# Performance work log

Measured on AMD Instinct MI355X. Metric: run time of the kernel, lower is better.

## Reference

```python
import jax, jax.numpy as jnp
import numpy as np

BS, N, D_IN, D_OUT, D_ENC, K = 8, 2048, 128, 128, 128, 2
EPS = 1e-5


def layer_norm(x, g, b):
    m = jnp.mean(x, axis=-1, keepdims=True)
    v = jnp.mean(jnp.square(x - m), axis=-1, keepdims=True)
    return (x - m) * jax.lax.rsqrt(v + EPS) * g + b


def setup_inputs() -> dict:
    key = jax.random.key(0)
    ks = jax.random.split(key, 12)
    s = lambda d: 1.0 / np.sqrt(d)
    return {
        "x": jax.random.normal(ks[0], (BS, N, D_IN), jnp.float32),
        "enc": jax.random.normal(ks[1], (BS, N, D_ENC), jnp.float32),
        "ff_enc_w": jax.random.uniform(ks[2], (D_IN, D_ENC), jnp.float32, -s(D_ENC), s(D_ENC)),
        "ff_enc_b": jax.random.uniform(ks[3], (D_IN,), jnp.float32, -s(D_ENC), s(D_ENC)),
        "ln1_g": jnp.ones((D_IN,), jnp.float32),
        "ln1_b": jnp.zeros((D_IN,), jnp.float32),
        "ln2_g": jnp.ones((D_IN,), jnp.float32),
        "ln2_b": jnp.zeros((D_IN,), jnp.float32),
        "ff0_w": jax.random.uniform(ks[4], (K, D_IN, D_IN), jnp.float32, -s(D_IN), s(D_IN)),
        "ff1_w": jax.random.uniform(ks[5], (K, D_OUT, D_IN), jnp.float32, -s(D_IN), s(D_IN)),
        "attn_w": jax.random.uniform(ks[6], (K, 2 * D_IN), jnp.float32, -s(2 * D_IN), s(2 * D_IN)),
    }


def reference(x, enc, ff_enc_w, ff_enc_b, ln1_g, ln1_b, ln2_g, ln2_b, ff0_w, ff1_w, attn_w):
    # x: [bs, n, d_in]; enc: [bs, n, d_enc]
    x = x + jnp.einsum("bne,de->bnd", enc, ff_enc_w) + ff_enc_b
    x_norm = layer_norm(x, ln1_g, ln1_b)
    k = ff0_w.shape[0]
    h_next = jnp.zeros(x.shape[:2] + (ff1_w.shape[1],), x.dtype)
    atten_agg = jnp.zeros(x.shape[:2] + (x.shape[1],), x.dtype)
    d = x.shape[-1]
    for i in range(k):
        h = jnp.einsum("bnd,ed->bne", x_norm, ff0_w[i])  # [bs,n,d]
        # cat(h_i, h_j) @ a  ==  h_i @ a1 + h_j @ a2  (additive-attention identity)
        s1 = h @ attn_w[i, :d]  # [bs,n]
        s2 = h @ attn_w[i, d:]  # [bs,n]
        e = jax.nn.leaky_relu(s1[:, :, None] + s2[:, None, :], negative_slope=0.01)
        atten = jax.nn.softmax(e, axis=2)  # [bs,n,n], softmax over j
        attentioned = jnp.einsum("bij,bjd->bid", atten, h) + x  # residual
        attentioned = layer_norm(attentioned, ln2_g, ln2_b)
        h_next = h_next + jax.nn.elu(jnp.einsum("bnd,od->bno", attentioned, ff1_w[i])) / k
        atten_agg = atten_agg + jax.lax.stop_gradient(atten) / k
    return (h_next, atten_agg)
```

## Files before the change

kernel.cpp:

```cpp
#include <hip/hip_runtime.h>
#include <hip/hip_bf16.h>
#include <math.h>

#define BSZ 8
#define NSEQ 2048
#define DD 128
#define ROWS (BSZ*NSEQ)
#define EPS 1e-5f

__device__ __forceinline__ float f4get(const float4& v, int i){
    return i==0 ? v.x : i==1 ? v.y : i==2 ? v.z : v.w;
}
__device__ __forceinline__ float eluf(float z){ return z > 0.f ? z : expm1f(z); }

__global__ __launch_bounds__(256) void k_transpose(
    const float* __restrict__ Wenc, const float* __restrict__ ff0,
    const float* __restrict__ ff1, float* __restrict__ Wt)
{
    __shared__ float t[32][33];
    const int m = blockIdx.x >> 4;
    const int tile = blockIdx.x & 15;
    const int ti = tile >> 2, tj = tile & 3;
    const float* src = (m == 0) ? Wenc
                     : (m <= 2) ? ff0 + (size_t)(m-1)*16384
                                : ff1 + (size_t)(m-3)*16384;
    float* dst = Wt + (size_t)m*16384;
    const int c = threadIdx.x & 31, r8 = threadIdx.x >> 5;
    #pragma unroll
    for (int p = 0; p < 4; ++p){
        int r = r8 + p*8;
        t[r][c] = src[(ti*32 + r)*128 + tj*32 + c];
    }
    __syncthreads();
    #pragma unroll
    for (int p = 0; p < 4; ++p){
        int r = r8 + p*8;
        dst[(tj*32 + r)*128 + ti*32 + c] = t[c][r];
    }
}

template<int MODE>
__global__ __launch_bounds__(256) void k_gemm(
    const float* __restrict__ A, const float* __restrict__ Bt,
    float* __restrict__ C,
    const float* __restrict__ P0, const float* __restrict__ P1,
    const float* __restrict__ P2, const float* __restrict__ P3,
    float* __restrict__ O1, float* __restrict__ O2)
{
    __shared__ float As[64][36];
    __shared__ float Bs[32][128];
    const int tid = threadIdx.x;
    const int tx = tid & 15, ty = tid >> 4;
    const int rowBase = blockIdx.x * 64;

    float acc[4][8];
    #pragma unroll
    for (int i = 0; i < 4; ++i)
        #pragma unroll
        for (int j = 0; j < 8; ++j) acc[i][j] = 0.f;

    for (int k0 = 0; k0 < 128; k0 += 32){
        {
            const int kk = tid & 31, rr = tid >> 5;
            #pragma unroll
            for (int p = 0; p < 8; ++p){
                int r = rr + p*8;
                As[r][kk] = A[(size_t)(rowBase + r)*128 + k0 + kk];
            }
        }
        {
            const int n = tid & 127, kk2 = tid >> 7;
            #pragma unroll
            for (int p = 0; p < 16; ++p){
                int kk = kk2 + p*2;
                Bs[kk][n] = Bt[(size_t)(k0 + kk)*128 + n];
            }
        }
        __syncthreads();
        #pragma unroll
        for (int kk4 = 0; kk4 < 32; kk4 += 4){
            float4 a[4];
            float4 b[4][2];
            #pragma unroll
            for (int rr = 0; rr < 4; ++rr)
                a[rr] = *(const float4*)&As[4*ty + rr][kk4];
            #pragma unroll
            for (int kk = 0; kk < 4; ++kk){
                b[kk][0] = *(const float4*)&Bs[kk4 + kk][8*tx];
                b[kk][1] = *(const float4*)&Bs[kk4 + kk][8*tx + 4];
            }
            #pragma unroll
            for (int kk = 0; kk < 4; ++kk){
                float bb[8] = {b[kk][0].x, b[kk][0].y, b[kk][0].z, b[kk][0].w,
                               b[kk][1].x, b[kk][1].y, b[kk][1].z, b[kk][1].w};
                #pragma unroll
                for (int rr = 0; rr < 4; ++rr){
                    float av = f4get(a[rr], kk);
                    #pragma unroll
                    for (int cc = 0; cc < 8; ++cc)
                        acc[rr][cc] += av * bb[cc];
                }
            }
        }
        __syncthreads();
    }

    const int c0 = 8*tx;
    if (MODE == 0){
        float4 be0 = *(const float4*)&P1[c0], be1 = *(const float4*)&P1[c0+4];
        float4 g0  = *(const float4*)&P2[c0], g1v = *(const float4*)&P2[c0+4];
        float4 bb0 = *(const float4*)&P3[c0], bb1 = *(const float4*)&P3[c0+4];
        #pragma unroll
        for (int rr = 0; rr < 4; ++rr){
            const size_t off = (size_t)(rowBase + 4*ty + rr)*128 + c0;
            float4 xi0 = *(const float4*)&P0[off];
            float4 xi1 = *(const float4*)&P0[off+4];
            float v[8];
            v[0]=acc[rr][0]+xi0.x+be0.x; v[1]=acc[rr][1]+xi0.y+be0.y;
            v[2]=acc[rr][2]+xi0.z+be0.z; v[3]=acc[rr][3]+xi0.w+be0.w;
            v[4]=acc[rr][4]+xi1.x+be1.x; v[5]=acc[rr][5]+xi1.y+be1.y;
            v[6]=acc[rr][6]+xi1.z+be1.z; v[7]=acc[rr][7]+xi1.w+be1.w;
            *(float4*)&C[off]   = make_float4(v[0],v[1],v[2],v[3]);
            *(float4*)&C[off+4] = make_float4(v[4],v[5],v[6],v[7]);
            float s = v[0]+v[1]+v[2]+v[3]+v[4]+v[5]+v[6]+v[7];
            #pragma unroll
            for (int m = 1; m < 16; m <<= 1) s += __shfl_xor(s, m, 64);
            float mean = s * (1.f/128.f);
            float q = 0.f;
            #pragma unroll
            for (int j = 0; j < 8; ++j){ float d = v[j]-mean; q += d*d; }
            #pragma unroll
            for (int m = 1; m < 16; m <<= 1) q += __shfl_xor(q, m, 64);
            float rstd = rsqrtf(q * (1.f/128.f) + EPS);
            float o[8];
            o[0]=(v[0]-mean)*rstd*g0.x+bb0.x; o[1]=(v[1]-mean)*rstd*g0.y+bb0.y;
            o[2]=(v[2]-mean)*rstd*g0.z+bb0.z; o[3]=(v[3]-mean)*rstd*g0.w+bb0.w;
            o[4]=(v[4]-mean)*rstd*g1v.x+bb1.x; o[5]=(v[5]-mean)*rstd*g1v.y+bb1.y;
            o[6]=(v[6]-mean)*rstd*g1v.z+bb1.z; o[7]=(v[7]-mean)*rstd*g1v.w+bb1.w;
            *(float4*)&O1[off]   = make_float4(o[0],o[1],o[2],o[3]);
            *(float4*)&O1[off+4] = make_float4(o[4],o[5],o[6],o[7]);
        }
    } else if (MODE == 1 || MODE == 4){
        float4 a10 = *(const float4*)&P1[c0],     a11 = *(const float4*)&P1[c0+4];
        float4 a20 = *(const float4*)&P1[128+c0], a21 = *(const float4*)&P1[128+c0+4];
        #pragma unroll
        for (int rr = 0; rr < 4; ++rr){
            const size_t off = (size_t)(rowBase + 4*ty + rr)*128 + c0;
            if (MODE == 1){
                *(float4*)&C[off]   = make_float4(acc[rr][0],acc[rr][1],acc[rr][2],acc[rr][3]);
                *(float4*)&C[off+4] = make_float4(acc[rr][4],acc[rr][5],acc[rr][6],acc[rr][7]);
            }
            float p1 = acc[rr][0]*a10.x+acc[rr][1]*a10.y+acc[rr][2]*a10.z+acc[rr][3]*a10.w
                     + acc[rr][4]*a11.x+acc[rr][5]*a11.y+acc[rr][6]*a11.z+acc[rr][7]*a11.w;
            float p2 = acc[rr][0]*a20.x+acc[rr][1]*a20.y+acc[rr][2]*a20.z+acc[rr][3]*a20.w
                     + acc[rr][4]*a21.x+acc[rr][5]*a21.y+acc[rr][6]*a21.z+acc[rr][7]*a21.w;
            #pragma unroll
            for (int m = 1; m < 16; m <<= 1){
                p1 += __shfl_xor(p1, m, 64);
                p2 += __shfl_xor(p2, m, 64);
            }
            if (tx == 0){
                O1[rowBase + 4*ty + rr] = p1;
                O2[rowBase + 4*ty + rr] = p2;
            }
        }
    } else if (MODE == 2){
        #pragma unroll
        for (int rr = 0; rr < 4; ++rr){
            const size_t off = (size_t)(rowBase + 4*ty + rr)*128 + c0;
            *(float4*)&C[off]   = make_float4(acc[rr][0],acc[rr][1],acc[rr][2],acc[rr][3]);
            *(float4*)&C[off+4] = make_float4(acc[rr][4],acc[rr][5],acc[rr][6],acc[rr][7]);
        }
    } else {
        #pragma unroll
        for (int rr = 0; rr < 4; ++rr){
            const size_t off = (size_t)(rowBase + 4*ty + rr)*128 + c0;
            float u[8];
            #pragma unroll
            for (int j = 0; j < 8; ++j) u[j] = 0.5f*eluf(acc[rr][j]);
            if (MODE == 3){
                float4 pa = *(const float4*)&C[off];
                float4 pb = *(const float4*)&C[off+4];
                u[0]+=pa.x; u[1]+=pa.y; u[2]+=pa.z; u[3]+=pa.w;
                u[4]+=pb.x; u[5]+=pb.y; u[6]+=pb.z; u[7]+=pb.w;
            }
            *(float4*)&C[off]   = make_float4(u[0],u[1],u[2],u[3]);
            *(float4*)&C[off+4] = make_float4(u[4],u[5],u[6],u[7]);
        }
    }
}

__global__ __launch_bounds__(1024) void k_sort(
    const float* __restrict__ s2k,
    float* __restrict__ s2s, int* __restrict__ perm,
    float* __restrict__ SEx, float* __restrict__ SFx,
    float* __restrict__ Eo, float* __restrict__ Fo,
    float* __restrict__ M2b)
{
    __shared__ float val[2048];
    __shared__ int   idx[2048];
    __shared__ float sa[2048], sb[2048], fa[2048], fb[2048];
    const int k = blockIdx.x >> 3, b = blockIdx.x & 7;
    const int t = threadIdx.x;
    const float* s2g = s2k + (size_t)k*ROWS + b*2048;
    float* s2so = s2s + k*16384 + b*2048;
    int*   permo = perm + k*16384 + b*2048;
    float* SExo = SEx + k*16392 + b*2049;
    float* SFxo = SFx + k*16392 + b*2049;
    float* Eok = Eo + (size_t)k*ROWS + b*2048;
    float* Fok = Fo + (size_t)k*ROWS + b*2048;

    for (int c = t; c < 2048; c += 1024){ val[c] = -s2g[c]; idx[c] = c; }
    __syncthreads();
    for (int kk = 2; kk <= 2048; kk <<= 1)
        for (int jj = kk >> 1; jj > 0; jj >>= 1){
            for (int c = t; c < 2048; c += 1024){
                int ixj = c ^ jj;
                if (ixj > c){
                    bool up = ((c & kk) == 0);
                    float av = val[c], bv = val[ixj];
                    if ((av > bv) == up){
                        val[c] = bv; val[ixj] = av;
                        int ia = idx[c]; idx[c] = idx[ixj]; idx[ixj] = ia;
                    }
                }
            }
            __syncthreads();
        }
    const float M2 = -val[0];
    for (int c = t; c < 2048; c += 1024){
        float sv = -val[c] - M2;
        sa[c] = expf(sv);
        fa[c] = expf(0.01f * sv);
    }
    __syncthreads();
    float *ss = sa, *sd = sb, *fs = fa, *fd = fb;
    for (int d = 1; d < 2048; d <<= 1){
        for (int c = t; c < 2048; c += 1024){
            sd[c] = ss[c] + (c >= d ? ss[c-d] : 0.f);
            fd[c] = fs[c] + (c >= d ? fs[c-d] : 0.f);
        }
        __syncthreads();
        float* tmp = ss; ss = sd; sd = tmp;
        tmp = fs; fs = fd; fd = tmp;
    }
    if (t == 0){ SExo[0] = 0.f; SFxo[0] = 0.f; M2b[k*8 + b] = M2; }
    for (int c = t; c < 2048; c += 1024){
        s2so[c]  = -val[c];
        permo[c] = idx[c];
        SExo[c + 1] = ss[c];
        SFxo[c + 1] = fs[c];
        float dv = s2g[c] - M2;
        Eok[c] = expf(dv);
        Fok[c] = expf(0.01f * dv);
    }
}

__global__ __launch_bounds__(256) void k_scanA(
    const float* __restrict__ h, const int* __restrict__ perm,
    const float* __restrict__ Eo, const float* __restrict__ Fo,
    float* __restrict__ PEc, float* __restrict__ PFc,
    float* __restrict__ PEt, float* __restrict__ PFt)
{
    const int b = blockIdx.x, ch = blockIdx.y;
    const int t = threadIdx.x;
    const bool isF = t >= 128;
    const int d = t & 127;
    const float* Wv = isF ? Fo : Eo;
    float* Pc = isF ? PFc : PEc;
    float* Pt = isF ? PFt : PEt;
    float acc = 0.f;
    const int c0 = ch * 128;
    #pragma unroll 4
    for (int c = c0; c < c0 + 128; ++c){
        int j = perm[b*2048 + c];
        float w = Wv[b*2048 + j];
        float hv = h[(size_t)(b*2048 + j)*128 + d];
        Pc[(size_t)(b*2048 + c)*128 + d] = acc;
        acc += w * hv;
    }
    Pt[(b*16 + ch)*128 + d] = acc;
}

__global__ __launch_bounds__(256) void k_scanB(
    const float* __restrict__ PEt, const float* __restrict__ PFt,
    float* __restrict__ PEo, float* __restrict__ PFo)
{
    const int b = blockIdx.x, t = threadIdx.x;
    const bool isF = t >= 128;
    const int d = t & 127;
    const float* Pt = isF ? PFt : PEt;
    float* Po = isF ? PFo : PEo;
    float acc = 0.f;
    Po[(b*17)*128 + d] = 0.f;
    for (int ch = 0; ch < 16; ++ch){
        acc += Pt[(b*16 + ch)*128 + d];
        Po[(b*17 + ch + 1)*128 + d] = acc;
    }
}

__global__ __launch_bounds__(256) void k_attn_pre(
    const float* __restrict__ x, const float* __restrict__ s1g,
    const float* __restrict__ s2s, const float* __restrict__ SEx, const float* __restrict__ SFx,
    const float* __restrict__ PEc, const float* __restrict__ PFc,
    const float* __restrict__ PEo, const float* __restrict__ PFo,
    const float* __restrict__ M2b,
    const float* __restrict__ g2, const float* __restrict__ b2,
    float* __restrict__ nout, float* __restrict__ Ap, float* __restrict__ Bp)
{
    const int tid = threadIdx.x;
    const int wv = tid >> 6, lane = tid & 63;
    const int row = blockIdx.x * 4 + wv;
    const int b = row >> 11;
    const float s1v = s1g[row];
    const float M2 = M2b[b];
    const float t0 = s1v + M2;
    const float m  = (t0 >= 0.f) ? t0 : 0.01f*t0;
    const float A  = expf(t0 - m);
    const float B  = expf(0.01f*t0 - m);
    int lo = 0, hi = 2048;
    while (lo < hi){
        int mid = (lo + hi) >> 1;
        if (s2s[b*2048 + mid] >= -s1v) lo = mid + 1; else hi = mid;
    }
    const int c = lo;
    const float ZE  = SEx[b*2049 + c];
    const float ZF  = SFx[b*2049 + c];
    const float ZFt = SFx[b*2049 + 2048];
    const float Z = A*ZE + B*(ZFt - ZF);
    if (lane == 0){ Ap[row] = A / Z; Bp[row] = B / Z; }
    const float rz = 1.f / Z;
    const int ch = c >> 7;
    const int d0 = lane, d1 = lane + 64;
    float pe0 = PEo[(b*17 + ch)*128 + d0], pe1 = PEo[(b*17 + ch)*128 + d1];
    float pf0 = PFo[(b*17 + ch)*128 + d0], pf1 = PFo[(b*17 + ch)*128 + d1];
    if (c < 2048){
        pe0 += PEc[(size_t)(b*2048 + c)*128 + d0];
        pe1 += PEc[(size_t)(b*2048 + c)*128 + d1];
        pf0 += PFc[(size_t)(b*2048 + c)*128 + d0];
        pf1 += PFc[(size_t)(b*2048 + c)*128 + d1];
    }
    const float pft0 = PFo[(b*17 + 16)*128 + d0], pft1 = PFo[(b*17 + 16)*128 + d1];
    float a0 = (A*pe0 + B*(pft0 - pf0))*rz + x[row*128 + d0];
    float a1 = (A*pe1 + B*(pft1 - pf1))*rz + x[row*128 + d1];
    float s = a0 + a1;
    #pragma unroll
    for (int mm = 32; mm; mm >>= 1) s += __shfl_xor(s, mm, 64);
    float mean = s * (1.f/128.f);
    float c0v = a0 - mean, c1v = a1 - mean;
    float q = c0v*c0v + c1v*c1v;
    #pragma unroll
    for (int mm = 32; mm; mm >>= 1) q += __shfl_xor(q, mm, 64);
    float rstd = rsqrtf(q * (1.f/128.f) + EPS);
    nout[row*128 + d0] = c0v*rstd*g2[d0] + b2[d0];
    nout[row*128 + d1] = c1v*rstd*g2[d1] + b2[d1];
}

__global__ __launch_bounds__(256) void k_agg(
    const float* __restrict__ s1_0, const float* __restrict__ s2_0,
    const float* __restrict__ E0, const float* __restrict__ F0,
    const float* __restrict__ Ap0, const float* __restrict__ Bp0,
    const float* __restrict__ s1_1, const float* __restrict__ s2_1,
    const float* __restrict__ E1, const float* __restrict__ F1,
    const float* __restrict__ Ap1, const float* __restrict__ Bp1,
    float* __restrict__ agg)
{
    __shared__ __align__(16) float s2a[2048], ea[2048], fa[2048];
    __shared__ __align__(16) float s2b[2048], eb[2048], fb[2048];
    const int b = blockIdx.x >> 6;
    const int tile = blockIdx.x & 63;
    const int t = threadIdx.x;
    for (int j = t; j < 2048; j += 256){
        s2a[j] = s2_0[b*2048 + j]; ea[j] = E0[b*2048 + j]; fa[j] = F0[b*2048 + j];
        s2b[j] = s2_1[b*2048 + j]; eb[j] = E1[b*2048 + j]; fb[j] = F1[b*2048 + j];
    }
    __syncthreads();
    for (int r = 0; r < 32; ++r){
        const int i = tile*32 + r;
        const int row = b*2048 + i;
        const float pa = Ap0[row], pb = Bp0[row], sa1 = s1_0[row];
        const float qa = Ap1[row], qb = Bp1[row], sb1 = s1_1[row];
        float4* outp = (float4*)(agg + (size_t)row * 2048);
        for (int j4 = t; j4 < 512; j4 += 256){
            float4 va  = ((const float4*)s2a)[j4];
            float4 vea = ((const float4*)ea )[j4];
            float4 vfa = ((const float4*)fa )[j4];
            float4 vb  = ((const float4*)s2b)[j4];
            float4 veb = ((const float4*)eb )[j4];
            float4 vfb = ((const float4*)fb )[j4];
            float4 o;
            o.x = 0.5f*(((sa1+va.x >= 0.f) ? pa*vea.x : pb*vfa.x) + ((sb1+vb.x >= 0.f) ? qa*veb.x : qb*vfb.x));
            o.y = 0.5f*(((sa1+va.y >= 0.f) ? pa*vea.y : pb*vfa.y) + ((sb1+vb.y >= 0.f) ? qa*veb.y : qb*vfb.y));
            o.z = 0.5f*(((sa1+va.z >= 0.f) ? pa*vea.z : pb*vfa.z) + ((sb1+vb.z >= 0.f) ? qa*veb.z : qb*vfb.z));
            o.w = 0.5f*(((sa1+va.w >= 0.f) ? pa*vea.w : pb*vfa.w) + ((sb1+vb.w >= 0.f) ? qa*veb.w : qb*vfb.w));
            outp[j4] = o;
        }
    }
}

extern "C" void kernel_launch(void* const* d_in, const int* in_sizes, int n_in,
                              void* d_out, int out_size, void* d_ws, size_t ws_size,
                              hipStream_t stream)
{
    const float* xin  = (const float*)d_in[0];
    const float* enc  = (const float*)d_in[1];
    const float* Wenc = (const float*)d_in[2];
    const float* benc = (const float*)d_in[3];
    const float* g1   = (const float*)d_in[4];
    const float* b1   = (const float*)d_in[5];
    const float* g2   = (const float*)d_in[6];
    const float* b2   = (const float*)d_in[7];
    const float* ff0  = (const float*)d_in[8];
    const float* ff1  = (const float*)d_in[9];
    const float* aw   = (const float*)d_in[10];

    float* out = (float*)d_out;
    float* agg = out + (size_t)ROWS * 128;

    const size_t R = ROWS, RD = (size_t)ROWS * 128;
    float* ws  = (float*)d_ws;
    float* Wt  = ws;
    float* x   = Wt + 5*16384;
    float* xn  = x + RD;
    float* h   = xn + RD;
    float* PEc = h + RD;
    float* PFc = PEc + RD;
    float* PEt = PFc + RD;
    float* PFt = PEt + 16384;
    float* PEo = PFt + 16384;
    float* PFo = PEo + 17408;
    float* s2s = PFo + 17408;
    int*   perm = (int*)(s2s + 2*16384);
    float* SEx = (float*)(perm + 2*16384);
    float* SFx = SEx + 2*16392;
    float* M2b = SFx + 2*16392;
    float* s1k = M2b + 16;
    float* s2k = s1k + 2*R;
    float* Ek  = s2k + 2*R;
    float* Fk  = Ek + 2*R;
    float* Apk = Fk + 2*R;
    float* Bpk = Apk + 2*R;

    k_transpose<<<80, 256, 0, stream>>>(Wenc, ff0, ff1, Wt);

    k_gemm<0><<<ROWS/64, 256, 0, stream>>>(enc, Wt, x, xin, benc, g1, b1, xn, nullptr);

    k_gemm<1><<<ROWS/64, 256, 0, stream>>>(xn, Wt + 16384, h, nullptr, aw, nullptr, nullptr,
                                           s1k, s2k);
    k_gemm<4><<<ROWS/64, 256, 0, stream>>>(xn, Wt + 2*16384, nullptr, nullptr, aw + 256,
                                           nullptr, nullptr, s1k + R, s2k + R);

    k_sort<<<16, 1024, 0, stream>>>(s2k, s2s, perm, SEx, SFx, Ek, Fk, M2b);

    for (int k = 0; k < 2; ++k){
        if (k == 1)
            k_gemm<2><<<ROWS/64, 256, 0, stream>>>(xn, Wt + 2*16384, h,
                                                   nullptr, nullptr, nullptr, nullptr,
                                                   nullptr, nullptr);
        k_scanA<<<dim3(BSZ, 16), 256, 0, stream>>>(h, perm + k*16384,
                                                   Ek + k*R, Fk + k*R,
                                                   PEc, PFc, PEt, PFt);
        k_scanB<<<BSZ, 256, 0, stream>>>(PEt, PFt, PEo, PFo);
        k_attn_pre<<<ROWS/4, 256, 0, stream>>>(x, s1k + k*R, s2s + k*16384,
                                               SEx + k*16392, SFx + k*16392,
                                               PEc, PFc, PEo, PFo, M2b + k*8,
                                               g2, b2, h, Apk + k*R, Bpk + k*R);
        if (k == 0)
            k_gemm<5><<<ROWS/64, 256, 0, stream>>>(h, Wt + 3*16384, out,
                                                   nullptr, nullptr, nullptr, nullptr,
                                                   nullptr, nullptr);
        else
            k_gemm<3><<<ROWS/64, 256, 0, stream>>>(h, Wt + 4*16384, out,
                                                   nullptr, nullptr, nullptr, nullptr,
                                                   nullptr, nullptr);
    }

    k_agg<<<BSZ*64, 256, 0, stream>>>(s1k, s2k, Ek, Fk, Apk, Bpk,
                                      s1k + R, s2k + R, Ek + R, Fk + R, Apk + R, Bpk + R,
                                      agg);
}
```

Before: 388.2 us.

## Shrink GEMM row tiles, merge both head projections, and finer-grained scan chunks

GEMM blocks now cover 32 rows instead of 64, doubling block count for better occupancy across CUs. The two per-head projection GEMMs (modes 1 and 4) are merged into one launch using a 2D grid indexed by head. The prefix-scan over sorted keys uses 64 chunks of 32 instead of 16 of 128, with permutation indices and weights staged in shared memory, increasing parallelism of the serial scan at the cost of a longer chunk-total scan in k_scanB.

```diff
diff --git a/kernel.cpp b/kernel.cpp
--- a/kernel.cpp
+++ b/kernel.cpp
@@ -7,6 +7,8 @@
 #define DD 128
 #define ROWS (BSZ*NSEQ)
 #define EPS 1e-5f
+#define CH 32
+#define NCH 64
 
 __device__ __forceinline__ float f4get(const float4& v, int i){
     return i==0 ? v.x : i==1 ? v.y : i==2 ? v.z : v.w;
@@ -47,15 +49,17 @@
     const float* __restrict__ P2, const float* __restrict__ P3,
     float* __restrict__ O1, float* __restrict__ O2)
 {
-    __shared__ float As[64][36];
+    __shared__ float As[32][36];
     __shared__ float Bs[32][128];
     const int tid = threadIdx.x;
     const int tx = tid & 15, ty = tid >> 4;
-    const int rowBase = blockIdx.x * 64;
-
-    float acc[4][8];
-    #pragma unroll
-    for (int i = 0; i < 4; ++i)
+    const int rowBase = blockIdx.x * 32;
+    const int ky = (MODE == 6) ? blockIdx.y : 0;
+    const float* Btk = Bt + (size_t)ky * 16384;
+
+    float acc[2][8];
+    #pragma unroll
+    for (int i = 0; i < 2; ++i)
         #pragma unroll
         for (int j = 0; j < 8; ++j) acc[i][j] = 0.f;
 
@@ -63,7 +67,7 @@
         {
             const int kk = tid & 31, rr = tid >> 5;
             #pragma unroll
-            for (int p = 0; p < 8; ++p){
+            for (int p = 0; p < 4; ++p){
                 int r = rr + p*8;
                 As[r][kk] = A[(size_t)(rowBase + r)*128 + k0 + kk];
             }
@@ -73,17 +77,15 @@
             #pragma unroll
             for (int p = 0; p < 16; ++p){
                 int kk = kk2 + p*2;
-                Bs[kk][n] = Bt[(size_t)(k0 + kk)*128 + n];
+                Bs[kk][n] = Btk[(size_t)(k0 + kk)*128 + n];
             }
         }
         __syncthreads();
         #pragma unroll
         for (int kk4 = 0; kk4 < 32; kk4 += 4){
-            float4 a[4];
+            float4 a0 = *(const float4*)&As[2*ty    ][kk4];
+            float4 a1 = *(const float4*)&As[2*ty + 1][kk4];
             float4 b[4][2];
-            #pragma unroll
-            for (int rr = 0; rr < 4; ++rr)
-                a[rr] = *(const float4*)&As[4*ty + rr][kk4];
             #pragma unroll
             for (int kk = 0; kk < 4; ++kk){
                 b[kk][0] = *(const float4*)&Bs[kk4 + kk][8*tx];
@@ -93,12 +95,11 @@
             for (int kk = 0; kk < 4; ++kk){
                 float bb[8] = {b[kk][0].x, b[kk][0].y, b[kk][0].z, b[kk][0].w,
                                b[kk][1].x, b[kk][1].y, b[kk][1].z, b[kk][1].w};
+                float av0 = f4get(a0, kk), av1 = f4get(a1, kk);
                 #pragma unroll
-                for (int rr = 0; rr < 4; ++rr){
-                    float av = f4get(a[rr], kk);
-                    #pragma unroll
-                    for (int cc = 0; cc < 8; ++cc)
-                        acc[rr][cc] += av * bb[cc];
+                for (int cc = 0; cc < 8; ++cc){
+                    acc[0][cc] += av0 * bb[cc];
+                    acc[1][cc] += av1 * bb[cc];
                 }
             }
         }
@@ -111,8 +112,8 @@
         float4 g0  = *(const float4*)&P2[c0], g1v = *(const float4*)&P2[c0+4];
         float4 bb0 = *(const float4*)&P3[c0], bb1 = *(const float4*)&P3[c0+4];
         #pragma unroll
-        for (int rr = 0; rr < 4; ++rr){
-            const size_t off = (size_t)(rowBase + 4*ty + rr)*128 + c0;
+        for (int rr = 0; rr < 2; ++rr){
+            const size_t off = (size_t)(rowBase + 2*ty + rr)*128 + c0;
             float4 xi0 = *(const float4*)&P0[off];
             float4 xi1 = *(const float4*)&P0[off+4];
             float v[8];
@@ -128,7 +129,7 @@
             float mean = s * (1.f/128.f);
             float q = 0.f;
             #pragma unroll
-            for (int j = 0; j < 8; ++j){ float d = v[j]-mean; q += d*d; }
+            for (int j = 0; j < 8; ++j){ float dd = v[j]-mean; q += dd*dd; }
             #pragma unroll
             for (int m = 1; m < 16; m <<= 1) q += __shfl_xor(q, m, 64);
             float rstd = rsqrtf(q * (1.f/128.f) + EPS);
@@ -140,13 +141,16 @@
             *(float4*)&O1[off]   = make_float4(o[0],o[1],o[2],o[3]);
             *(float4*)&O1[off+4] = make_float4(o[4],o[5],o[6],o[7]);
         }
-    } else if (MODE == 1 || MODE == 4){
-        float4 a10 = *(const float4*)&P1[c0],     a11 = *(const float4*)&P1[c0+4];
-        float4 a20 = *(const float4*)&P1[128+c0], a21 = *(const float4*)&P1[128+c0+4];
-        #pragma unroll
-        for (int rr = 0; rr < 4; ++rr){
-            const size_t off = (size_t)(rowBase + 4*ty + rr)*128 + c0;
-            if (MODE == 1){
+    } else if (MODE == 6){
+        const float* P1k = P1 + ky*256;
+        float* O1k = O1 + (size_t)ky*ROWS;
+        float* O2k = O2 + (size_t)ky*ROWS;
+        float4 a10 = *(const float4*)&P1k[c0],     a11 = *(const float4*)&P1k[c0+4];
+        float4 a20 = *(const float4*)&P1k[128+c0], a21 = *(const float4*)&P1k[128+c0+4];
+        #pragma unroll
+        for (int rr = 0; rr < 2; ++rr){
+            const size_t off = (size_t)(rowBase + 2*ty + rr)*128 + c0;
+            if (ky == 0){
                 *(float4*)&C[off]   = make_float4(acc[rr][0],acc[rr][1],acc[rr][2],acc[rr][3]);
                 *(float4*)&C[off+4] = make_float4(acc[rr][4],acc[rr][5],acc[rr][6],acc[rr][7]);
             }
@@ -160,21 +164,21 @@
                 p2 += __shfl_xor(p2, m, 64);
             }
             if (tx == 0){
-                O1[rowBase + 4*ty + rr] = p1;
-                O2[rowBase + 4*ty + rr] = p2;
+                O1k[rowBase + 2*ty + rr] = p1;
+                O2k[rowBase + 2*ty + rr] = p2;
             }
         }
     } else if (MODE == 2){
         #pragma unroll
-        for (int rr = 0; rr < 4; ++rr){
-            const size_t off = (size_t)(rowBase + 4*ty + rr)*128 + c0;
+        for (int rr = 0; rr < 2; ++rr){
+            const size_t off = (size_t)(rowBase + 2*ty + rr)*128 + c0;
             *(float4*)&C[off]   = make_float4(acc[rr][0],acc[rr][1],acc[rr][2],acc[rr][3]);
             *(float4*)&C[off+4] = make_float4(acc[rr][4],acc[rr][5],acc[rr][6],acc[rr][7]);
         }
     } else {
         #pragma unroll
-        for (int rr = 0; rr < 4; ++rr){
-            const size_t off = (size_t)(rowBase + 4*ty + rr)*128 + c0;
+        for (int rr = 0; rr < 2; ++rr){
+            const size_t off = (size_t)(rowBase + 2*ty + rr)*128 + c0;
             float u[8];
             #pragma unroll
             for (int j = 0; j < 8; ++j) u[j] = 0.5f*eluf(acc[rr][j]);
@@ -262,24 +266,29 @@
     float* __restrict__ PEc, float* __restrict__ PFc,
     float* __restrict__ PEt, float* __restrict__ PFt)
 {
+    __shared__ int js[CH];
+    __shared__ float wE[CH], wF[CH];
     const int b = blockIdx.x, ch = blockIdx.y;
     const int t = threadIdx.x;
+    const int c0 = ch * CH;
+    if (t < CH) js[t] = perm[b*2048 + c0 + t];
+    __syncthreads();
+    if (t < CH) wE[t] = Eo[b*2048 + js[t]];
+    else if (t < 2*CH) wF[t-CH] = Fo[b*2048 + js[t-CH]];
+    __syncthreads();
     const bool isF = t >= 128;
     const int d = t & 127;
-    const float* Wv = isF ? Fo : Eo;
+    const float* wv = isF ? wF : wE;
     float* Pc = isF ? PFc : PEc;
     float* Pt = isF ? PFt : PEt;
     float acc = 0.f;
-    const int c0 = ch * 128;
-    #pragma unroll 4
-    for (int c = c0; c < c0 + 128; ++c){
-        int j = perm[b*2048 + c];
-        float w = Wv[b*2048 + j];
-        float hv = h[(size_t)(b*2048 + j)*128 + d];
-        Pc[(size_t)(b*2048 + c)*128 + d] = acc;
-        acc += w * hv;
-    }
-    Pt[(b*16 + ch)*128 + d] = acc;
+    #pragma unroll
+    for (int i = 0; i < CH; ++i){
+        float hv = h[(size_t)(b*2048 + js[i])*128 + d];
+        Pc[(size_t)(b*2048 + c0 + i)*128 + d] = acc;
+        acc += wv[i] * hv;
+    }
+    Pt[(b*NCH + ch)*128 + d] = acc;
 }
 
 __global__ __launch_bounds__(256) void k_scanB(
@@ -292,10 +301,11 @@
     const float* Pt = isF ? PFt : PEt;
     float* Po = isF ? PFo : PEo;
     float acc = 0.f;
-    Po[(b*17)*128 + d] = 0.f;
-    for (int ch = 0; ch < 16; ++ch){
-        acc += Pt[(b*16 + ch)*128 + d];
-        Po[(b*17 + ch + 1)*128 + d] = acc;
+    Po[(b*(NCH+1))*128 + d] = 0.f;
+    #pragma unroll
+    for (int ch = 0; ch < NCH; ++ch){
+        acc += Pt[(b*NCH + ch)*128 + d];
+        Po[(b*(NCH+1) + ch + 1)*128 + d] = acc;
     }
 }
 
@@ -330,17 +340,17 @@
     const float Z = A*ZE + B*(ZFt - ZF);
     if (lane == 0){ Ap[row] = A / Z; Bp[row] = B / Z; }
     const float rz = 1.f / Z;
-    const int ch = c >> 7;
+    const int ch = c >> 5;
     const int d0 = lane, d1 = lane + 64;
-    float pe0 = PEo[(b*17 + ch)*128 + d0], pe1 = PEo[(b*17 + ch)*128 + d1];
-    float pf0 = PFo[(b*17 + ch)*128 + d0], pf1 = PFo[(b*17 + ch)*128 + d1];
+    float pe0 = PEo[(b*(NCH+1) + ch)*128 + d0], pe1 = PEo[(b*(NCH+1) + ch)*128 + d1];
+    float pf0 = PFo[(b*(NCH+1) + ch)*128 + d0], pf1 = PFo[(b*(NCH+1) + ch)*128 + d1];
     if (c < 2048){
         pe0 += PEc[(size_t)(b*2048 + c)*128 + d0];
         pe1 += PEc[(size_t)(b*2048 + c)*128 + d1];
         pf0 += PFc[(size_t)(b*2048 + c)*128 + d0];
         pf1 += PFc[(size_t)(b*2048 + c)*128 + d1];
     }
-    const float pft0 = PFo[(b*17 + 16)*128 + d0], pft1 = PFo[(b*17 + 16)*128 + d1];
+    const float pft0 = PFo[(b*(NCH+1) + NCH)*128 + d0], pft1 = PFo[(b*(NCH+1) + NCH)*128 + d1];
     float a0 = (A*pe0 + B*(pft0 - pf0))*rz + x[row*128 + d0];
     float a1 = (A*pe1 + B*(pft1 - pf1))*rz + x[row*128 + d1];
     float s = a0 + a1;
@@ -426,10 +436,10 @@
     float* PEc = h + RD;
     float* PFc = PEc + RD;
     float* PEt = PFc + RD;
-    float* PFt = PEt + 16384;
-    float* PEo = PFt + 16384;
-    float* PFo = PEo + 17408;
-    float* s2s = PFo + 17408;
+    float* PFt = PEt + 8*NCH*128;
+    float* PEo = PFt + 8*NCH*128;
+    float* PFo = PEo + 8*(NCH+1)*128;
+    float* s2s = PFo + 8*(NCH+1)*128;
     int*   perm = (int*)(s2s + 2*16384);
     float* SEx = (float*)(perm + 2*16384);
     float* SFx = SEx + 2*16392;
@@ -443,34 +453,33 @@
 
     k_transpose<<<80, 256, 0, stream>>>(Wenc, ff0, ff1, Wt);
 
-    k_gemm<0><<<ROWS/64, 256, 0, stream>>>(enc, Wt, x, xin, benc, g1, b1, xn, nullptr);
-
-    k_gemm<1><<<ROWS/64, 256, 0, stream>>>(xn, Wt + 16384, h, nullptr, aw, nullptr, nullptr,
-                                           s1k, s2k);
-    k_gemm<4><<<ROWS/64, 256, 0, stream>>>(xn, Wt + 2*16384, nullptr, nullptr, aw + 256,
-                                           nullptr, nullptr, s1k + R, s2k + R);
+    k_gemm<0><<<ROWS/32, 256, 0, stream>>>(enc, Wt, x, xin, benc, g1, b1, xn, nullptr);
+
+    k_gemm<6><<<dim3(ROWS/32, 2), 256, 0, stream>>>(xn, Wt + 16384, h,
+                                                    nullptr, aw, nullptr, nullptr,
+                                                    s1k, s2k);
 
     k_sort<<<16, 1024, 0, stream>>>(s2k, s2s, perm, SEx, SFx, Ek, Fk, M2b);
 
     for (int k = 0; k < 2; ++k){
         if (k == 1)
-            k_gemm<2><<<ROWS/64, 256, 0, stream>>>(xn, Wt + 2*16384, h,
+            k_gemm<2><<<ROWS/32, 256, 0, stream>>>(xn, Wt + 2*16384, h,
                                                    nullptr, nullptr, nullptr, nullptr,
                                                    nullptr, nullptr);
-        k_scanA<<<dim3(BSZ, 16), 256, 0, stream>>>(h, perm + k*16384,
-                                                   Ek + k*R, Fk + k*R,
-                                                   PEc, PFc, PEt, PFt);
+        k_scanA<<<dim3(BSZ, NCH), 256, 0, stream>>>(h, perm + k*16384,
+                                                    Ek + k*R, Fk + k*R,
+                                                    PEc, PFc, PEt, PFt);
         k_scanB<<<BSZ, 256, 0, stream>>>(PEt, PFt, PEo, PFo);
         k_attn_pre<<<ROWS/4, 256, 0, stream>>>(x, s1k + k*R, s2s + k*16384,
                                                SEx + k*16392, SFx + k*16392,
                                                PEc, PFc, PEo, PFo, M2b + k*8,
                                                g2, b2, h, Apk + k*R, Bpk + k*R);
         if (k == 0)
-            k_gemm<5><<<ROWS/64, 256, 0, stream>>>(h, Wt + 3*16384, out,
+            k_gemm<5><<<ROWS/32, 256, 0, stream>>>(h, Wt + 3*16384, out,
                                                    nullptr, nullptr, nullptr, nullptr,
                                                    nullptr, nullptr);
         else
-            k_gemm<3><<<ROWS/64, 256, 0, stream>>>(h, Wt + 4*16384, out,
+            k_gemm<3><<<ROWS/32, 256, 0, stream>>>(h, Wt + 4*16384, out,
                                                    nullptr, nullptr, nullptr, nullptr,
                                                    nullptr, nullptr);
     }
```

New measurement: 366.4 us. 1.06x faster.
